# Optimization experiments

Hardware: AMD Instinct MI355X
Metric: run time of the kernel (lower is better)

## Reference

```python
import jax, jax.numpy as jnp
import numpy as np

RADIUS = 5
KERNEL_SIZE = 2 * RADIUS - 1  # 9
PAD = KERNEL_SIZE // 2        # 4
H, W = 2048, 2048


def make_distance_kernel():
    center = RADIUS - 1
    y, x = jnp.meshgrid(jnp.arange(KERNEL_SIZE), jnp.arange(KERNEL_SIZE), indexing='ij')
    d = jnp.sqrt((x - center).astype(jnp.float32) ** 2 + (y - center).astype(jnp.float32) ** 2)
    return d.at[center, center].set(0.0)


def setup_inputs() -> dict:
    key = jax.random.key(0)
    target = (jax.random.uniform(key, (5, H, W)) < 0.15).astype(jnp.float32)
    distance_kernel = make_distance_kernel()
    return {"target": target, "distance_kernel": distance_kernel}


def _contour_weights(target, kernel):
    combined = (target.sum(axis=0) > 0).astype(jnp.float32)          # [H, W]
    padded = jnp.pad(combined, PAD, mode='edge')                      # replicate pad
    min_d = jnp.full_like(combined, jnp.inf)
    inf = jnp.float32(jnp.inf)
    for i in range(KERNEL_SIZE):
        for j in range(KERNEL_SIZE):
            if i == PAD and j == PAD:
                continue
            shifted = padded[i:i + H, j:j + W]
            diff = (shifted != combined).astype(jnp.float32)
            dist = jnp.where(diff > 0, kernel[i, j] / (diff + 1e-10), inf)
            min_d = jnp.minimum(min_d, dist)
    return jnp.where(min_d < inf, 1.0 / (min_d + 1e-10), 0.0)


def reference(target, distance_kernel):
    feature_weight = target.sum(axis=0)                               # [H, W]
    contour = _contour_weights(target, distance_kernel)
    weights = (feature_weight + contour) ** 2
    weights = (weights - weights.min()) / (weights.max() - weights.min() + 1e-10)
    return weights * (target.sum(axis=0) > 0).astype(jnp.float32)
```

## Files before the change

### kernel.cpp

```cpp
#include <hip/hip_runtime.h>
#include <stdint.h>

#define HH 2048
#define WW 2048
#define NPIX (HH*WW)
#define MROW (WW/32)
#define TSX 64
#define TSY 32
#define NBLK ((WW/TSX)*(HH/TSY))

__global__ __launch_bounds__(256) void fw_kernel(
    const float* __restrict__ target, uint16_t* __restrict__ fwnib,
    uint32_t* __restrict__ mask)
{
    __shared__ uint8_t nib[256];
    const int t = threadIdx.x;
    const int i = blockIdx.x * 256 + t;
    const float4* t4 = (const float4*)target;
    float4 a = t4[i];
    float4 b = t4[(NPIX/4) + i];
    float4 c = t4[2*(NPIX/4) + i];
    float4 d = t4[3*(NPIX/4) + i];
    float4 e = t4[4*(NPIX/4) + i];
    uint32_t f0 = (uint32_t)(a.x + b.x + c.x + d.x + e.x);
    uint32_t f1 = (uint32_t)(a.y + b.y + c.y + d.y + e.y);
    uint32_t f2 = (uint32_t)(a.z + b.z + c.z + d.z + e.z);
    uint32_t f3 = (uint32_t)(a.w + b.w + c.w + d.w + e.w);
    fwnib[i] = (uint16_t)(f0 | (f1 << 4) | (f2 << 8) | (f3 << 12));
    nib[t] = (uint8_t)((f0 ? 1u : 0u) | (f1 ? 2u : 0u) | (f2 ? 4u : 0u) | (f3 ? 8u : 0u));
    __syncthreads();
    if (t < 32) {
        const uint8_t* p = nib + t * 8;
        uint32_t w = 0;
        #pragma unroll
        for (int k = 0; k < 8; ++k) w |= (uint32_t)p[k] << (4 * k);
        mask[blockIdx.x * 32 + t] = w;
    }
}

__global__ __launch_bounds__(256) void contour_kernel(
    const uint16_t* __restrict__ fwnib, const uint32_t* __restrict__ mask,
    const float* __restrict__ dk,
    uint8_t* __restrict__ wcode, float* __restrict__ pmin, float* __restrict__ pmax)
{
    __shared__ uint32_t maskw[TSY + 8][4];
    __shared__ uint8_t  lutm2[512];
    __shared__ float    inv_ext[65];
    __shared__ float    redmn[4], redmx[4];

    const int t   = threadIdx.x;
    const int gx0 = blockIdx.x * TSX;
    const int gy0 = blockIdx.y * TSY;
    const int rl  = t >> 3;
    const int xg  = t & 7;
    const int gy  = gy0 + rl;
    const int gxb = gx0 + 8 * xg;

    const int w0 = gx0 >> 5;
    if (t < (TSY + 8) * 4) {
        int hr = t >> 2, wc = t & 3;
        int hgy = gy0 - 4 + hr; hgy = min(max(hgy, 0), HH - 1);
        const uint32_t* rowp = mask + hgy * MROW;
        int wi = w0 - 1 + wc;
        uint32_t v;
        if (wi < 0)            v = (rowp[0] & 1u) ? 0xFFFFFFFFu : 0u;
        else if (wi > MROW-1)  v = (rowp[MROW-1] >> 31) ? 0xFFFFFFFFu : 0u;
        else                   v = rowp[wi];
        maskw[hr][wc] = v;
    }
    const uint32_t fwd = *(const uint32_t*)((const uint8_t*)fwnib + gy * (WW/2) + (gxb >> 1));
    for (int idx = t; idx < 512; idx += 256) {
        uint32_t rev = __builtin_bitreverse32((uint32_t)idx) >> 23;
        uint32_t g = ((((uint32_t)idx | rev) >> 4) & 0x1Fu) | 0x100u;
        uint32_t mk = (uint32_t)__builtin_ctz(g);
        lutm2[idx] = (uint8_t)(mk * mk);
    }
    if (t < 65) inv_ext[t] = 0.0f;
    __syncthreads();
    if (t < 81) {
        int iy = t / 9, jx = t - (t / 9) * 9;
        int dy = iy - 4, dx = jx - 4;
        int d2 = dy * dy + dx * dx;
        if (d2 != 0) inv_ext[d2] = 1.0f / (dk[t] / (1.0f + 1e-10f) + 1e-10f);
    }
    __syncthreads();

    const int pos  = 8 * xg + 28;
    const int wsel = pos >> 5;
    const uint32_t sh = (uint32_t)(pos & 31);
    uint32_t wrow[9];
    #pragma unroll
    for (int k = 0; k < 9; ++k) {
        uint64_t v = (((uint64_t)maskw[rl + k][wsel + 1]) << 32) | maskw[rl + k][wsel];
        wrow[k] = (uint32_t)(v >> sh);
    }
    uint32_t orx[4], andx[4];
    #pragma unroll
    for (int k = 1; k <= 4; ++k) {
        orx[k-1]  = wrow[4 - k] | wrow[4 + k];
        andx[k-1] = wrow[4 - k] & wrow[4 + k];
    }
    float lmn = __int_as_float(0x7F800000);
    float lmx = 0.0f;
    uint32_t outb0 = 0, outb1 = 0;
    #pragma unroll
    for (int j = 0; j < 8; ++j) {
        uint32_t craw = (wrow[4] >> (4 + j)) & 1u;
        uint32_t cm = 0u - craw;
        uint32_t x0 = ((wrow[4] ^ cm) >> j) & 0x1FFu;
        uint32_t d2m = (uint32_t)lutm2[x0];
        #pragma unroll
        for (int k = 1; k <= 4; ++k) {
            uint32_t sel = craw ? andx[k-1] : orx[k-1];
            uint32_t x = ((sel ^ cm) >> j) & 0x1FFu;
            uint32_t d2 = (uint32_t)lutm2[x] + (uint32_t)(k * k);
            d2m = min(d2m, d2);
        }
        float contour = inv_ext[d2m];
        uint32_t enc = (d2m > 32u) ? 26u : d2m;
        uint32_t fwj = (fwd >> (4 * j)) & 0xFu;
        uint32_t code = ((enc - 1u) << 3) | fwj;
        if (j < 4) outb0 |= code << (8 * j);
        else       outb1 |= code << (8 * (j - 4));
        float wv = (float)fwj + contour;
        wv = wv * wv;
        lmn = fminf(lmn, wv);
        lmx = fmaxf(lmx, wv);
    }
    uint2 ob; ob.x = outb0; ob.y = outb1;
    *(uint2*)(wcode + gy * WW + gxb) = ob;

    #pragma unroll
    for (int off = 32; off > 0; off >>= 1) {
        lmn = fminf(lmn, __shfl_xor(lmn, off));
        lmx = fmaxf(lmx, __shfl_xor(lmx, off));
    }
    if ((t & 63) == 0) { redmn[t >> 6] = lmn; redmx[t >> 6] = lmx; }
    __syncthreads();
    if (t == 0) {
        float mn = fminf(fminf(redmn[0], redmn[1]), fminf(redmn[2], redmn[3]));
        float mx = fmaxf(fmaxf(redmx[0], redmx[1]), fmaxf(redmx[2], redmx[3]));
        int bid = blockIdx.y * gridDim.x + blockIdx.x;
        pmin[bid] = mn;
        pmax[bid] = mx;
    }
}

__global__ __launch_bounds__(256) void norm_kernel(
    const uint8_t* __restrict__ wcode, const float* __restrict__ dk,
    const float* __restrict__ pmin, const float* __restrict__ pmax,
    float* __restrict__ out)
{
    __shared__ float ct[33];
    __shared__ float wlut[256];
    __shared__ float smn[4], smx[4];
    const int t = threadIdx.x;

    if (t < 33) ct[t] = 0.0f;
    const float4* pn4 = (const float4*)pmin;
    const float4* px4 = (const float4*)pmax;
    float4 a = pn4[t * 2], b = pn4[t * 2 + 1];
    float4 c = px4[t * 2], d = px4[t * 2 + 1];
    __syncthreads();
    if (t < 81) {
        int iy = t / 9, jx = t - (t / 9) * 9;
        int dy = iy - 4, dx = jx - 4;
        int d2 = dy * dy + dx * dx;
        if (d2 != 0) ct[d2] = 1.0f / (dk[t] / (1.0f + 1e-10f) + 1e-10f);
    }
    __syncthreads();
    {
        float wv = (float)(t & 7) + ct[(t >> 3) + 1];
        wlut[t] = wv * wv;
    }
    float mn = fminf(fminf(fminf(a.x, a.y), fminf(a.z, a.w)),
                     fminf(fminf(b.x, b.y), fminf(b.z, b.w)));
    float mx = fmaxf(fmaxf(fmaxf(c.x, c.y), fmaxf(c.z, c.w)),
                     fmaxf(fmaxf(d.x, d.y), fmaxf(d.z, d.w)));
    #pragma unroll
    for (int off = 32; off > 0; off >>= 1) {
        mn = fminf(mn, __shfl_xor(mn, off));
        mx = fmaxf(mx, __shfl_xor(mx, off));
    }
    if ((t & 63) == 0) { smn[t >> 6] = mn; smx[t >> 6] = mx; }
    __syncthreads();
    mn = fminf(fminf(smn[0], smn[1]), fminf(smn[2], smn[3]));
    mx = fmaxf(fmaxf(smx[0], smx[1]), fmaxf(smx[2], smx[3]));
    const float rden = 1.0f / (mx - mn + 1e-10f);

    const int i = blockIdx.x * 256 + t;
    uint2 cb = ((const uint2*)wcode)[i];
    uint32_t b0 = cb.x, b1 = cb.y;
    float4 o0, o1;
    o0.x = (b0 & 7u)         ? (wlut[b0 & 0xFFu] - mn) * rden         : 0.0f;
    o0.y = ((b0 >> 8) & 7u)  ? (wlut[(b0 >> 8) & 0xFFu] - mn) * rden  : 0.0f;
    o0.z = ((b0 >> 16) & 7u) ? (wlut[(b0 >> 16) & 0xFFu] - mn) * rden : 0.0f;
    o0.w = ((b0 >> 24) & 7u) ? (wlut[b0 >> 24] - mn) * rden           : 0.0f;
    o1.x = (b1 & 7u)         ? (wlut[b1 & 0xFFu] - mn) * rden         : 0.0f;
    o1.y = ((b1 >> 8) & 7u)  ? (wlut[(b1 >> 8) & 0xFFu] - mn) * rden  : 0.0f;
    o1.z = ((b1 >> 16) & 7u) ? (wlut[(b1 >> 16) & 0xFFu] - mn) * rden : 0.0f;
    o1.w = ((b1 >> 24) & 7u) ? (wlut[b1 >> 24] - mn) * rden           : 0.0f;
    ((float4*)out)[i * 2]     = o0;
    ((float4*)out)[i * 2 + 1] = o1;
}

extern "C" void kernel_launch(void* const* d_in, const int* in_sizes, int n_in,
                              void* d_out, int out_size, void* d_ws, size_t ws_size,
                              hipStream_t stream)
{
    const float* target = (const float*)d_in[0];
    const float* dk     = (const float*)d_in[1];
    float* out = (float*)d_out;

    uint8_t* wsb = (uint8_t*)d_ws;
    uint16_t* fwnib = (uint16_t*)wsb;
    uint8_t*  wcode = wsb + NPIX/2;
    uint32_t* mask  = (uint32_t*)(wsb + NPIX/2 + NPIX);
    float*    pmin  = (float*)(wsb + NPIX/2 + NPIX + NPIX/8);
    float*    pmax  = pmin + NBLK;

    fw_kernel<<<NPIX / 4 / 256, 256, 0, stream>>>(target, fwnib, mask);

    dim3 gridB(WW / TSX, HH / TSY);
    contour_kernel<<<gridB, 256, 0, stream>>>(fwnib, mask, dk, wcode, pmin, pmax);

    norm_kernel<<<NPIX / 8 / 256, 256, 0, stream>>>(wcode, dk, pmin, pmax, out);
}
```

Before: 36.13 us.

## Resolve distance-1/2 contour pixels with bitwise ops, fall back for rest

Computes, with word-wide bit logic, which pixels have a differing neighbour at squared distance 1 or 2, and writes their codes and min/max contributions directly. Only the unresolved pixels go through the full 9x9 search, now done in a wave-uniform loop that computes the distance lookup arithmetically instead of through a shared-memory table. With about 15% foreground per channel most pixels should resolve early. The cost is a divergent slow path that runs whenever any lane in a wave has an unresolved pixel.

```diff
diff --git a/kernel.cpp b/kernel.cpp
--- a/kernel.cpp
+++ b/kernel.cpp
@@ -8,6 +8,13 @@
 #define TSX 64
 #define TSY 32
 #define NBLK ((WW/TSX)*(HH/TSY))
+
+__device__ __forceinline__ uint32_t m2gadget(uint32_t x) {
+    uint32_t rev = __builtin_bitreverse32(x) >> 23;
+    uint32_t g = (((x | rev) >> 4) & 0x1Fu) | 0x100u;
+    uint32_t mk = (uint32_t)__builtin_ctz(g);
+    return mk * mk;
+}
 
 __global__ __launch_bounds__(256) void fw_kernel(
     const float* __restrict__ target, uint16_t* __restrict__ fwnib,
@@ -44,7 +51,6 @@
     uint8_t* __restrict__ wcode, float* __restrict__ pmin, float* __restrict__ pmax)
 {
     __shared__ uint32_t maskw[TSY + 8][4];
-    __shared__ uint8_t  lutm2[512];
     __shared__ float    inv_ext[65];
     __shared__ float    redmn[4], redmx[4];
 
@@ -69,12 +75,6 @@
         maskw[hr][wc] = v;
     }
     const uint32_t fwd = *(const uint32_t*)((const uint8_t*)fwnib + gy * (WW/2) + (gxb >> 1));
-    for (int idx = t; idx < 512; idx += 256) {
-        uint32_t rev = __builtin_bitreverse32((uint32_t)idx) >> 23;
-        uint32_t g = ((((uint32_t)idx | rev) >> 4) & 0x1Fu) | 0x100u;
-        uint32_t mk = (uint32_t)__builtin_ctz(g);
-        lutm2[idx] = (uint8_t)(mk * mk);
-    }
     if (t < 65) inv_ext[t] = 0.0f;
     __syncthreads();
     if (t < 81) {
@@ -94,39 +94,69 @@
         uint64_t v = (((uint64_t)maskw[rl + k][wsel + 1]) << 32) | maskw[rl + k][wsel];
         wrow[k] = (uint32_t)(v >> sh);
     }
-    uint32_t orx[4], andx[4];
-    #pragma unroll
-    for (int k = 1; k <= 4; ++k) {
-        orx[k-1]  = wrow[4 - k] | wrow[4 + k];
-        andx[k-1] = wrow[4 - k] & wrow[4 + k];
-    }
-    float lmn = __int_as_float(0x7F800000);
-    float lmx = 0.0f;
-    uint32_t outb0 = 0, outb1 = 0;
+
+    const uint32_t C  = (wrow[4] >> 4) & 0xFFu;
+    const uint32_t or1  = wrow[3] | wrow[5];
+    const uint32_t and1 = wrow[3] & wrow[5];
+    uint32_t or_ab  = ((wrow[4] >> 3) | (wrow[4] >> 5)) | (or1 >> 4);
+    uint32_t and_ab = ((wrow[4] >> 3) & (wrow[4] >> 5)) & (and1 >> 4);
+    uint32_t P1 = ((C & ~and_ab) | (~C & or_ab)) & 0xFFu;
+    uint32_t or_c  = (or1 >> 3) | (or1 >> 5);
+    uint32_t and_c = (and1 >> 3) & (and1 >> 5);
+    uint32_t P2 = (((C & ~and_c) | (~C & or_c)) & 0xFFu) & ~P1;
+    uint32_t unres = 0xFFu & ~(P1 | P2);
+
+    uint32_t u0 = fwd & 0x0F0F0F0Fu;
+    uint32_t u1 = (fwd >> 4) & 0x0F0F0F0Fu;
+    uint32_t outb0 = (u0 & 0xFFu) | ((u1 & 0xFFu) << 8)
+                   | ((u0 & 0xFF00u) << 8) | ((u1 & 0xFF00u) << 16);
+    uint32_t outb1 = ((u0 >> 16) & 0xFFu) | (((u1 >> 16) & 0xFFu) << 8)
+                   | (((u0 >> 24) & 0xFFu) << 16) | (((u1 >> 24) & 0xFFu) << 24);
+    outb0 |= (((P2 & 0xFu)  * 0x00204081u) & 0x01010101u) << 3;
+    outb1 |= (((P2 >> 4)    * 0x00204081u) & 0x01010101u) << 3;
+
+    const float c1 = inv_ext[1], c2 = inv_ext[2];
+    const float FINF = __int_as_float(0x7F800000);
+    float lmn = FINF, lmx = 0.0f;
     #pragma unroll
     for (int j = 0; j < 8; ++j) {
-        uint32_t craw = (wrow[4] >> (4 + j)) & 1u;
-        uint32_t cm = 0u - craw;
-        uint32_t x0 = ((wrow[4] ^ cm) >> j) & 0x1FFu;
-        uint32_t d2m = (uint32_t)lutm2[x0];
-        #pragma unroll
-        for (int k = 1; k <= 4; ++k) {
-            uint32_t sel = craw ? andx[k-1] : orx[k-1];
-            uint32_t x = ((sel ^ cm) >> j) & 0x1FFu;
-            uint32_t d2 = (uint32_t)lutm2[x] + (uint32_t)(k * k);
-            d2m = min(d2m, d2);
+        float fwf = (float)((fwd >> (4 * j)) & 0xFu);
+        float ctr = ((P1 >> j) & 1u) ? c1 : (((P2 >> j) & 1u) ? c2 : 0.0f);
+        float wv = fwf + ctr;
+        wv = wv * wv;
+        bool u = ((unres >> j) & 1u) != 0u;
+        lmn = fminf(lmn, u ? FINF : wv);
+        lmx = fmaxf(lmx, u ? 0.0f : wv);
+    }
+
+    uint32_t un = unres;
+    while (__any(un != 0u)) {
+        if (un) {
+            int j = __builtin_ctz(un);
+            un &= un - 1u;
+            uint32_t craw = (C >> j) & 1u;
+            uint32_t cm = 0u - craw;
+            uint32_t d2m = m2gadget(((wrow[4] ^ cm) >> j) & 0x1FFu);
+            #pragma unroll
+            for (int k = 1; k <= 4; ++k) {
+                uint32_t sel = craw ? (wrow[4 - k] & wrow[4 + k])
+                                    : (wrow[4 - k] | wrow[4 + k]);
+                uint32_t x = ((sel ^ cm) >> j) & 0x1FFu;
+                d2m = min(d2m, m2gadget(x) + (uint32_t)(k * k));
+            }
+            float contour = inv_ext[d2m];
+            uint32_t enc = (d2m > 32u) ? 26u : d2m;
+            uint32_t val = (enc - 1u) << 3;
+            if (j < 4) outb0 |= val << (8 * j);
+            else       outb1 |= val << (8 * (j - 4));
+            float fwf = (float)((fwd >> (4 * j)) & 0xFu);
+            float wv = fwf + contour;
+            wv = wv * wv;
+            lmn = fminf(lmn, wv);
+            lmx = fmaxf(lmx, wv);
         }
-        float contour = inv_ext[d2m];
-        uint32_t enc = (d2m > 32u) ? 26u : d2m;
-        uint32_t fwj = (fwd >> (4 * j)) & 0xFu;
-        uint32_t code = ((enc - 1u) << 3) | fwj;
-        if (j < 4) outb0 |= code << (8 * j);
-        else       outb1 |= code << (8 * (j - 4));
-        float wv = (float)fwj + contour;
-        wv = wv * wv;
-        lmn = fminf(lmn, wv);
-        lmx = fmaxf(lmx, wv);
-    }
+    }
+
     uint2 ob; ob.x = outb0; ob.y = outb1;
     *(uint2*)(wcode + gy * WW + gxb) = ob;
 
```

New measurement: 35.33 us. 1.02x faster.
